# Optimization experiments

Measured on AMD Instinct MI355X. Metric: run time of the kernel, lower is better.

The kernel has to match this reference:

```python
import jax, jax.numpy as jnp
import numpy as np

BN_EPS = 1e-5
STRIDE = 12          # ACCENT_DOWNSAMPLE_STRIDE
NQ = 8               # ACCENT_VQ_QUANTIZERS
K = 256              # ACCENT_VQ_CODEBOOK_SIZE
VQ_D = 16            # ACCENT_VQ_DIM
EMB = 128            # ACCENT_EMBEDDING_DIM


def conv1d(x, w, b, stride=1, padding=0):
    # x: (B, Cin, T), w: (Cout, Cin, Kw)
    y = jax.lax.conv_general_dilated(
        x, w, window_strides=(stride,), padding=[(padding, padding)],
        dimension_numbers=("NCW", "OIW", "NCW"))
    return y + b[None, :, None]


def batchnorm(x, gamma, beta, mean, var):
    # eval-mode BatchNorm1d over channel dim
    inv = jax.lax.rsqrt(var + BN_EPS)
    return (x - mean[None, :, None]) * (inv * gamma)[None, :, None] + beta[None, :, None]


def setup_inputs() -> dict:
    key = jax.random.key(0)
    ks = jax.random.split(key, 12)
    C = 256
    d = {
        "mel_spectrogram": jax.random.normal(ks[0], (16, 80, 4096), jnp.float32),
        "w1": jax.random.normal(ks[1], (C, 80, 5), jnp.float32) * 0.05,
        "b1": jnp.zeros((C,), jnp.float32),
        "g1": jnp.ones((C,), jnp.float32),
        "be1": jnp.zeros((C,), jnp.float32),
        "m1": jax.random.normal(ks[2], (C,), jnp.float32) * 0.1,
        "v1": jax.random.uniform(ks[3], (C,), jnp.float32, 0.5, 1.5),
        "w2": jax.random.normal(ks[4], (C, C, 5), jnp.float32) * 0.03,
        "b2": jnp.zeros((C,), jnp.float32),
        "g2": jnp.ones((C,), jnp.float32),
        "be2": jnp.zeros((C,), jnp.float32),
        "m2": jax.random.normal(ks[5], (C,), jnp.float32) * 0.1,
        "v2": jax.random.uniform(ks[6], (C,), jnp.float32, 0.5, 1.5),
        "wd": jax.random.normal(ks[7], (EMB, C, 2 * STRIDE), jnp.float32) * 0.02,
        "bd": jnp.zeros((EMB,), jnp.float32),
        "wp": jax.random.normal(ks[8], (VQ_D, EMB, 1), jnp.float32) * 0.1,
        "bp": jnp.zeros((VQ_D,), jnp.float32),
        "codebooks": jax.random.normal(ks[9], (NQ, K, VQ_D), jnp.float32) * 0.3,
    }
    return d


def reference(mel_spectrogram, w1, b1, g1, be1, m1, v1,
              w2, b2, g2, be2, m2, v2, wd, bd, wp, bp, codebooks):
    # CNN stack
    x = jax.nn.relu(batchnorm(conv1d(mel_spectrogram, w1, b1, 1, 2), g1, be1, m1, v1))
    x = jax.nn.relu(batchnorm(conv1d(x, w2, b2, 1, 2), g2, be2, m2, v2))
    # Downsample conv: kernel=24, stride=12, pad=6
    e_a_unq = conv1d(x, wd, bd, STRIDE, STRIDE // 2)          # (B, 128, T')
    z = conv1d(e_a_unq, wp, bp, 1, 0)                          # (B, 16, T')
    # RVQ: 8 sequential cdist-argmin-subtract steps
    r = jnp.transpose(z, (0, 2, 1))                            # (B, T', 16)
    idx_list = []
    for q in range(NQ):
        cb = codebooks[q]                                      # (K, 16)
        # squared euclidean distances (B, T', K)
        d = (jnp.sum(r * r, -1, keepdims=True)
             - 2.0 * jnp.einsum("btd,kd->btk", r, cb)
             + jnp.sum(cb * cb, -1))
        idx = jnp.argmin(d, axis=-1)                           # (B, T')
        idx_list.append(idx)
        r = r - cb[idx]                                        # residual update
    indices = jnp.stack(idx_list, axis=0)                      # (NQ, B, T')
    return e_a_unq, indices
```

## Files before the change

kernel.cpp:

```cpp
#include <hip/hip_runtime.h>
#include <math.h>

#define B_    16
#define BCH   4
#define T_    4096
#define C_    256
#define CIN1  80
#define EMB   128
#define TP    341
#define NPOS  (B_*TP)
#define NQ_   8
#define KCB   256
#define BN_EPS 1e-5

__global__ __launch_bounds__(256) void prep_f64(
    const float* __restrict__ w1, const float* __restrict__ w2,
    const float* __restrict__ wd,
    const float* __restrict__ b1, const float* __restrict__ g1,
    const float* __restrict__ be1, const float* __restrict__ m1,
    const float* __restrict__ v1,
    const float* __restrict__ b2, const float* __restrict__ g2,
    const float* __restrict__ be2, const float* __restrict__ m2,
    const float* __restrict__ v2,
    const float* __restrict__ wp, const float* __restrict__ bp,
    double* __restrict__ w1t, double* __restrict__ w2t, double* __restrict__ wdt,
    double* __restrict__ a1, double* __restrict__ bt1,
    double* __restrict__ a2, double* __restrict__ bt2,
    double* __restrict__ wpd, double* __restrict__ bpd)
{
    int j = blockIdx.x * 256 + threadIdx.x;
    if (j < 256*24*128) wdt[j] = (double)wd[(size_t)(j & 127) * 6144 + (j >> 7)];
    if (j < 256*5*256)  w2t[j] = (double)w2[(size_t)(j & 255) * 1280 + (j >> 8)];
    if (j < 80*5*256)   w1t[j] = (double)w1[(size_t)(j & 255) * 400 + (j >> 8)];
    if (j < 16*128)     wpd[j] = (double)wp[j];
    if (j < 16)         bpd[j] = (double)bp[j];
    if (j < 256) {
        double inv1 = 1.0 / sqrt((double)v1[j] + BN_EPS);
        double s1 = (double)g1[j] * inv1;
        a1[j]  = s1;
        bt1[j] = ((double)b1[j] - (double)m1[j]) * s1 + (double)be1[j];
        double inv2 = 1.0 / sqrt((double)v2[j] + BN_EPS);
        double s2 = (double)g2[j] * inv2;
        a2[j]  = s2;
        bt2[j] = ((double)b2[j] - (double)m2[j]) * s2 + (double)be2[j];
    }
}

__device__ __forceinline__ int swz_pair(int col) {
    int bw = col >> 1;
    return ((bw ^ ((bw >> 3) & 7)) << 1);
}
__device__ __forceinline__ int swz_scalar(int col) {
    int bw = col >> 1;
    return (((bw ^ ((bw >> 3) & 7)) << 1) | (col & 1));
}

template<int CIN, typename Tin>
__global__ __launch_bounds__(256) void conv5_bn_relu_f64(
    const Tin* __restrict__ in,
    const double* __restrict__ wt,
    const double* __restrict__ alpha, const double* __restrict__ beta,
    double* __restrict__ out)
{
    const int b   = blockIdx.z;
    const int co0 = blockIdx.y * 64;
    const int t0  = blockIdx.x * 128;
    const int tid = threadIdx.x;
    const int tcol = tid & 15;
    const int trow = tid >> 4;

    __shared__ double xs[8][136];
    __shared__ double wsh[40][64];

    double acc[4][8];
    #pragma unroll
    for (int i = 0; i < 4; ++i)
        #pragma unroll
        for (int j = 0; j < 8; ++j) acc[i][j] = 0.0;

    for (int c0 = 0; c0 < CIN; c0 += 8) {
        for (int i = tid; i < 8 * 132; i += 256) {
            int ci = i / 132, col = i % 132;
            int t = t0 - 2 + col;
            double v = 0.0;
            if (t >= 0 && t < T_) v = (double)in[((size_t)(b * CIN + c0 + ci)) * T_ + t];
            xs[ci][swz_scalar(col)] = v;
        }
        for (int i = tid; i < 40 * 64; i += 256) {
            int r = i >> 6, co = i & 63;
            wsh[r][co] = wt[(size_t)(c0 * 5 + r) * 256 + co0 + co];
        }
        __syncthreads();

        #pragma unroll
        for (int ci = 0; ci < 8; ++ci) {
            double xv[12];
            #pragma unroll
            for (int m = 0; m < 6; ++m) {
                double2 v = *(const double2*)&xs[ci][swz_pair(tcol * 8 + 2 * m)];
                xv[2 * m] = v.x; xv[2 * m + 1] = v.y;
            }
            #pragma unroll
            for (int k = 0; k < 5; ++k) {
                double w0 = wsh[ci * 5 + k][trow * 4 + 0];
                double w1v = wsh[ci * 5 + k][trow * 4 + 1];
                double w2v = wsh[ci * 5 + k][trow * 4 + 2];
                double w3v = wsh[ci * 5 + k][trow * 4 + 3];
                #pragma unroll
                for (int j = 0; j < 8; ++j) {
                    double xq = xv[j + k];
                    acc[0][j] = fma(w0, xq, acc[0][j]);
                    acc[1][j] = fma(w1v, xq, acc[1][j]);
                    acc[2][j] = fma(w2v, xq, acc[2][j]);
                    acc[3][j] = fma(w3v, xq, acc[3][j]);
                }
            }
        }
        __syncthreads();
    }

    const int cobase = co0 + trow * 4;
    const int tg = t0 + tcol * 8;
    #pragma unroll
    for (int i = 0; i < 4; ++i) {
        double a = alpha[cobase + i], bt = beta[cobase + i];
        size_t base = ((size_t)(b * C_ + cobase + i)) * T_ + tg;
        #pragma unroll
        for (int j = 0; j < 8; ++j) {
            double y = fma(acc[i][j], a, bt);
            out[base + j] = y > 0.0 ? y : 0.0;
        }
    }
}

__global__ __launch_bounds__(256) void convd_f64_v6(
    const double* __restrict__ x2,
    const double* __restrict__ wdt,
    double* __restrict__ parts,
    int nb, int nsplit, int cis)
{
    const int bz  = blockIdx.z;
    const int s   = bz % nsplit;
    const int b   = bz / nsplit;
    const int tp0 = blockIdx.x * 64;
    const int tid = threadIdx.x;
    const int tcol = tid & 15;
    const int crow = tid >> 4;

    __shared__ double xs2[2][24][66];
    __shared__ double wsh[48][128];

    double acc[8][4];
    #pragma unroll
    for (int i = 0; i < 8; ++i)
        #pragma unroll
        for (int j = 0; j < 4; ++j) acc[i][j] = 0.0;

    const int tbase = tp0 * 12 - 6;
    const int ci_begin = s * cis;

    for (int c0 = ci_begin; c0 < ci_begin + cis; c0 += 2) {
        for (int i = tid; i < 2 * 780; i += 256) {
            int ci = i / 780, c = i % 780;
            int t = tbase + c;
            double v = (t >= 0 && t < T_)
                ? x2[((size_t)(b * 256 + c0 + ci)) * T_ + t] : 0.0;
            int tp = c / 12, kp = c % 12;
            xs2[ci][kp][tp] = v;
            if (tp >= 1) xs2[ci][kp + 12][tp - 1] = v;
        }
        for (int i = tid; i < 48 * 128; i += 256) {
            int r = i >> 7, c = i & 127;
            wsh[r][c] = wdt[(size_t)(c0 * 24 + r) * 128 + c];
        }
        __syncthreads();

        const double* xb = &xs2[0][0][0] + tcol;
        const double* wb = &wsh[0][0] + crow * 8;
        #pragma unroll
        for (int ci = 0; ci < 2; ++ci) {
            #pragma unroll
            for (int k = 0; k < 24; ++k) {
                double wv[8], xv[4];
                #pragma unroll
                for (int i = 0; i < 8; ++i) wv[i] = wb[(ci * 24 + k) * 128 + i];
                #pragma unroll
                for (int j = 0; j < 4; ++j) xv[j] = xb[(ci * 24 + k) * 66 + 16 * j];
                #pragma unroll
                for (int i = 0; i < 8; ++i)
                    #pragma unroll
                    for (int j = 0; j < 4; ++j)
                        acc[i][j] = fma(wv[i], xv[j], acc[i][j]);
            }
        }
        __syncthreads();
    }

    #pragma unroll
    for (int i = 0; i < 8; ++i) {
        int co = crow * 8 + i;
        #pragma unroll
        for (int j = 0; j < 4; ++j) {
            int tp = tp0 + tcol + 16 * j;
            if (tp < TP)
                parts[(((size_t)s * nb + b) * EMB + co) * TP + tp] = acc[i][j];
        }
    }
}

__global__ __launch_bounds__(256) void convd_combine(
    const double* __restrict__ parts,
    const float* __restrict__ bd,
    double* __restrict__ ed,
    float* __restrict__ e_out,
    int nb, int b_off, int nsplit)
{
    int idx = blockIdx.x * 256 + threadIdx.x;
    int total = nb * EMB * TP;
    if (idx >= total) return;
    int b_local = idx / (EMB * TP);
    int rem = idx % (EMB * TP);
    int co = rem / TP;
    size_t stride = (size_t)nb * EMB * TP;
    double y = 0.0;
    for (int s = 0; s < nsplit; ++s)
        y += parts[(size_t)s * stride + idx];
    y += (double)bd[co];
    size_t o = (size_t)(b_off + b_local) * EMB * TP + rem;
    ed[o] = y;
    e_out[o] = (float)y;
}

__global__ __launch_bounds__(128) void zproj_f64(
    const double* __restrict__ ed,
    const double* __restrict__ wpd,
    const double* __restrict__ bpd,
    double* __restrict__ z)
{
    const int b = blockIdx.y;
    const int t = blockIdx.x * 128 + threadIdx.x;
    __shared__ double wps[16][128];
    for (int i = threadIdx.x; i < 16 * 128; i += 128)
        wps[i >> 7][i & 127] = wpd[i];
    __syncthreads();
    if (t >= TP) return;
    double acc[16];
    #pragma unroll
    for (int v = 0; v < 16; ++v) acc[v] = bpd[v];
    for (int co = 0; co < 128; ++co) {
        double x = ed[((size_t)(b * EMB + co)) * TP + t];
        #pragma unroll
        for (int v = 0; v < 16; ++v) acc[v] = fma(x, wps[v][co], acc[v]);
    }
    #pragma unroll
    for (int v = 0; v < 16; ++v)
        z[((size_t)(b * TP + t)) * 16 + v] = acc[v];
}

__global__ __launch_bounds__(256) void rvq_f64_v2(
    const double* __restrict__ z,
    const float* __restrict__ cb,
    float* __restrict__ out_idx)
{
    const int pos = blockIdx.x;
    const int tid = threadIdx.x;
    const int lane = tid & 63;
    const int wv = tid >> 6;

    __shared__ double r[16];
    __shared__ double wd_s[4];
    __shared__ int wi_s[4];
    __shared__ int best_s;

    if (tid < 16) r[tid] = z[(size_t)pos * 16 + tid];
    __syncthreads();

    for (int q = 0; q < NQ_; ++q) {
        const float* c = cb + ((size_t)(q * KCB) + tid) * 16;
        double d = 0.0;
        #pragma unroll
        for (int i = 0; i < 16; ++i) {
            double diff = r[i] - (double)c[i];
            d = fma(diff, diff, d);
        }
        int idx = tid;
        #pragma unroll
        for (int sft = 32; sft > 0; sft >>= 1) {
            double d2 = __shfl_down(d, sft, 64);
            int i2 = __shfl_down(idx, sft, 64);
            if (d2 < d || (d2 == d && i2 < idx)) { d = d2; idx = i2; }
        }
        if (lane == 0) { wd_s[wv] = d; wi_s[wv] = idx; }
        __syncthreads();
        if (tid == 0) {
            double bd_ = wd_s[0]; int bi = wi_s[0];
            #pragma unroll
            for (int w = 1; w < 4; ++w) {
                if (wd_s[w] < bd_ || (wd_s[w] == bd_ && wi_s[w] < bi)) {
                    bd_ = wd_s[w]; bi = wi_s[w];
                }
            }
            best_s = bi;
            out_idx[(size_t)q * NPOS + pos] = (float)bi;
        }
        __syncthreads();
        int best = best_s;
        if (tid < 16)
            r[tid] = r[tid] - (double)cb[((size_t)(q * KCB) + best) * 16 + tid];
        __syncthreads();
    }
}

extern "C" void kernel_launch(void* const* d_in, const int* in_sizes, int n_in,
                              void* d_out, int out_size, void* d_ws, size_t ws_size,
                              hipStream_t stream) {
    const float* mel = (const float*)d_in[0];
    const float* w1  = (const float*)d_in[1];
    const float* b1  = (const float*)d_in[2];
    const float* g1  = (const float*)d_in[3];
    const float* be1 = (const float*)d_in[4];
    const float* m1  = (const float*)d_in[5];
    const float* v1  = (const float*)d_in[6];
    const float* w2  = (const float*)d_in[7];
    const float* b2  = (const float*)d_in[8];
    const float* g2  = (const float*)d_in[9];
    const float* be2 = (const float*)d_in[10];
    const float* m2  = (const float*)d_in[11];
    const float* v2  = (const float*)d_in[12];
    const float* wd  = (const float*)d_in[13];
    const float* bd  = (const float*)d_in[14];
    const float* wp  = (const float*)d_in[15];
    const float* bp  = (const float*)d_in[16];
    const float* cb  = (const float*)d_in[17];

    const int nb = 8;
    const int ngrp = B_ / nb;

    const size_t x1_bytes    = (size_t)BCH * C_ * T_ * 8;
    const size_t x2_bytes    = (size_t)nb * C_ * T_ * 8;
    const size_t fixed_bytes = x2_bytes + (size_t)80*5*256*8 + (size_t)256*5*256*8
                             + (size_t)256*24*128*8 + 4*2048 + 16384 + 256
                             + (size_t)16 * EMB * TP * 8
                             + (size_t)16 * TP * 16 * 8
                             + 16384;
    auto parts_bytes = [&](int ns) -> size_t {
        return (size_t)ns * nb * EMB * TP * 8;
    };
    auto need = [&](int ns) -> size_t {
        size_t shared = x1_bytes > parts_bytes(ns) ? x1_bytes : parts_bytes(ns);
        return shared + fixed_bytes;
    };
    int nsplit = (ws_size >= need(16)) ? 16 : 8;
    const int cis = 256 / nsplit;
    const size_t shared_bytes =
        x1_bytes > parts_bytes(nsplit) ? x1_bytes : parts_bytes(nsplit);

    char* ws = (char*)d_ws;
    size_t off = 0;
    auto alloc = [&](size_t bytes) -> char* {
        char* p = ws + off;
        off = (off + bytes + 255) & ~(size_t)255;
        return p;
    };
    char* shared = alloc(shared_bytes);
    double* x1d  = (double*)shared;
    double* parts= (double*)shared;
    double* x2d  = (double*)alloc(x2_bytes);
    double* w1td = (double*)alloc((size_t)80*5*256*8);
    double* w2td = (double*)alloc((size_t)256*5*256*8);
    double* wdtd = (double*)alloc((size_t)256*24*128*8);
    double* a1d  = (double*)alloc(2048);
    double* bt1d = (double*)alloc(2048);
    double* a2d  = (double*)alloc(2048);
    double* bt2d = (double*)alloc(2048);
    double* wpd  = (double*)alloc(16*128*8);
    double* bpd  = (double*)alloc(16*8);
    double* ed   = (double*)alloc((size_t)16 * EMB * TP * 8);
    double* zd   = (double*)alloc((size_t)16 * TP * 16 * 8);

    float* e_out   = (float*)d_out;
    float* idx_out = (float*)d_out + (size_t)B_ * EMB * TP;

    prep_f64<<<3072, 256, 0, stream>>>(w1, w2, wd, b1, g1, be1, m1, v1,
                                       b2, g2, be2, m2, v2, wp, bp,
                                       w1td, w2td, wdtd, a1d, bt1d, a2d, bt2d,
                                       wpd, bpd);

    const int comb_blocks = (nb * EMB * TP + 255) / 256;
    for (int g = 0; g < ngrp; ++g) {
        for (int ch = 0; ch < nb / BCH; ++ch) {
            int ch_abs = g * (nb / BCH) + ch;
            const float* mel_c = mel + (size_t)ch_abs * BCH * CIN1 * T_;
            conv5_bn_relu_f64<CIN1, float><<<dim3(32, 4, BCH), 256, 0, stream>>>(
                mel_c, w1td, a1d, bt1d, x1d);
            conv5_bn_relu_f64<C_, double><<<dim3(32, 4, BCH), 256, 0, stream>>>(
                x1d, w2td, a2d, bt2d, x2d + (size_t)ch * BCH * C_ * T_);
        }
        convd_f64_v6<<<dim3(6, 1, nb * nsplit), 256, 0, stream>>>(
            x2d, wdtd, parts, nb, nsplit, cis);
        convd_combine<<<comb_blocks, 256, 0, stream>>>(parts, bd, ed, e_out,
                                                       nb, g * nb, nsplit);
    }
    zproj_f64<<<dim3(3, 16), 128, 0, stream>>>(ed, wpd, bpd, zd);
    rvq_f64_v2<<<NPOS, 256, 0, stream>>>(zd, cb, idx_out);
}
```

Baseline: 1.876 ms.

## Keep weights in fp32, drop intermediate ed buffer, batch conv launches by workspace

Conv and projection weights now stay fp32 in global memory and are widened to double only when loaded into shared memory. w1 is read directly without a pre-transpose pass. The combine step writes reduced results in place into the partials buffer, and the z-projection then runs per group from that buffer, so the separate ed array is gone. When the workspace is large enough, each conv launch covers 8 batches instead of 4, and div/mod by 12 is replaced with a multiply-shift. The aim is less memory traffic, smaller prep work and fewer launches, at the cost of uncoalesced w1 loads and more complex workspace aliasing.

```diff
diff --git a/kernel.cpp b/kernel.cpp
--- a/kernel.cpp
+++ b/kernel.cpp
@@ -2,7 +2,6 @@
 #include <math.h>
 
 #define B_    16
-#define BCH   4
 #define T_    4096
 #define C_    256
 #define CIN1  80
@@ -13,27 +12,21 @@
 #define KCB   256
 #define BN_EPS 1e-5
 
-__global__ __launch_bounds__(256) void prep_f64(
-    const float* __restrict__ w1, const float* __restrict__ w2,
-    const float* __restrict__ wd,
+__global__ __launch_bounds__(256) void prep_v7(
+    const float* __restrict__ w2, const float* __restrict__ wd,
     const float* __restrict__ b1, const float* __restrict__ g1,
     const float* __restrict__ be1, const float* __restrict__ m1,
     const float* __restrict__ v1,
     const float* __restrict__ b2, const float* __restrict__ g2,
     const float* __restrict__ be2, const float* __restrict__ m2,
     const float* __restrict__ v2,
-    const float* __restrict__ wp, const float* __restrict__ bp,
-    double* __restrict__ w1t, double* __restrict__ w2t, double* __restrict__ wdt,
+    float* __restrict__ w2t, float* __restrict__ wdt,
     double* __restrict__ a1, double* __restrict__ bt1,
-    double* __restrict__ a2, double* __restrict__ bt2,
-    double* __restrict__ wpd, double* __restrict__ bpd)
+    double* __restrict__ a2, double* __restrict__ bt2)
 {
     int j = blockIdx.x * 256 + threadIdx.x;
-    if (j < 256*24*128) wdt[j] = (double)wd[(size_t)(j & 127) * 6144 + (j >> 7)];
-    if (j < 256*5*256)  w2t[j] = (double)w2[(size_t)(j & 255) * 1280 + (j >> 8)];
-    if (j < 80*5*256)   w1t[j] = (double)w1[(size_t)(j & 255) * 400 + (j >> 8)];
-    if (j < 16*128)     wpd[j] = (double)wp[j];
-    if (j < 16)         bpd[j] = (double)bp[j];
+    if (j < 256*24*128) wdt[j] = wd[(size_t)(j & 127) * 6144 + (j >> 7)];
+    if (j < 256*5*256)  w2t[j] = w2[(size_t)(j & 255) * 1280 + (j >> 8)];
     if (j < 256) {
         double inv1 = 1.0 / sqrt((double)v1[j] + BN_EPS);
         double s1 = (double)g1[j] * inv1;
@@ -55,10 +48,10 @@
     return (((bw ^ ((bw >> 3) & 7)) << 1) | (col & 1));
 }
 
-template<int CIN, typename Tin>
+template<int CIN, typename Tin, bool TR>
 __global__ __launch_bounds__(256) void conv5_bn_relu_f64(
     const Tin* __restrict__ in,
-    const double* __restrict__ wt,
+    const float* __restrict__ wt,
     const double* __restrict__ alpha, const double* __restrict__ beta,
     double* __restrict__ out)
 {
@@ -88,7 +81,10 @@
         }
         for (int i = tid; i < 40 * 64; i += 256) {
             int r = i >> 6, co = i & 63;
-            wsh[r][co] = wt[(size_t)(c0 * 5 + r) * 256 + co0 + co];
+            float wv;
+            if (TR) wv = wt[(size_t)(c0 * 5 + r) * 256 + co0 + co];
+            else    wv = wt[(size_t)(co0 + co) * (CIN * 5) + c0 * 5 + r];
+            wsh[r][co] = (double)wv;
         }
         __syncthreads();
 
@@ -135,7 +131,7 @@
 
 __global__ __launch_bounds__(256) void convd_f64_v6(
     const double* __restrict__ x2,
-    const double* __restrict__ wdt,
+    const float* __restrict__ wdt,
     double* __restrict__ parts,
     int nb, int nsplit, int cis)
 {
@@ -161,17 +157,19 @@
 
     for (int c0 = ci_begin; c0 < ci_begin + cis; c0 += 2) {
         for (int i = tid; i < 2 * 780; i += 256) {
-            int ci = i / 780, c = i % 780;
+            int ci = (i >= 780) ? 1 : 0;
+            int c = i - ci * 780;
             int t = tbase + c;
             double v = (t >= 0 && t < T_)
                 ? x2[((size_t)(b * 256 + c0 + ci)) * T_ + t] : 0.0;
-            int tp = c / 12, kp = c % 12;
+            int tp = (c * 43691) >> 19;
+            int kp = c - tp * 12;
             xs2[ci][kp][tp] = v;
             if (tp >= 1) xs2[ci][kp + 12][tp - 1] = v;
         }
         for (int i = tid; i < 48 * 128; i += 256) {
             int r = i >> 7, c = i & 127;
-            wsh[r][c] = wdt[(size_t)(c0 * 24 + r) * 128 + c];
+            wsh[r][c] = (double)wdt[(size_t)(c0 * 24 + r) * 128 + c];
         }
         __syncthreads();
 
@@ -209,44 +207,42 @@
 }
 
 __global__ __launch_bounds__(256) void convd_combine(
-    const double* __restrict__ parts,
+    double* __restrict__ parts,
     const float* __restrict__ bd,
-    double* __restrict__ ed,
     float* __restrict__ e_out,
     int nb, int b_off, int nsplit)
 {
     int idx = blockIdx.x * 256 + threadIdx.x;
     int total = nb * EMB * TP;
     if (idx >= total) return;
-    int b_local = idx / (EMB * TP);
     int rem = idx % (EMB * TP);
     int co = rem / TP;
+    int b_local = idx / (EMB * TP);
     size_t stride = (size_t)nb * EMB * TP;
     double y = 0.0;
     for (int s = 0; s < nsplit; ++s)
         y += parts[(size_t)s * stride + idx];
     y += (double)bd[co];
-    size_t o = (size_t)(b_off + b_local) * EMB * TP + rem;
-    ed[o] = y;
-    e_out[o] = (float)y;
+    parts[idx] = y;
+    e_out[(size_t)b_off * EMB * TP + idx] = (float)y;
 }
 
 __global__ __launch_bounds__(128) void zproj_f64(
     const double* __restrict__ ed,
-    const double* __restrict__ wpd,
-    const double* __restrict__ bpd,
+    const float* __restrict__ wp,
+    const float* __restrict__ bp,
     double* __restrict__ z)
 {
     const int b = blockIdx.y;
     const int t = blockIdx.x * 128 + threadIdx.x;
     __shared__ double wps[16][128];
     for (int i = threadIdx.x; i < 16 * 128; i += 128)
-        wps[i >> 7][i & 127] = wpd[i];
+        wps[i >> 7][i & 127] = (double)wp[i];
     __syncthreads();
     if (t >= TP) return;
     double acc[16];
     #pragma unroll
-    for (int v = 0; v < 16; ++v) acc[v] = bpd[v];
+    for (int v = 0; v < 16; ++v) acc[v] = (double)bp[v];
     for (int co = 0; co < 128; ++co) {
         double x = ed[((size_t)(b * EMB + co)) * TP + t];
         #pragma unroll
@@ -335,25 +331,24 @@
 
     const int nb = 8;
     const int ngrp = B_ / nb;
-
-    const size_t x1_bytes    = (size_t)BCH * C_ * T_ * 8;
-    const size_t x2_bytes    = (size_t)nb * C_ * T_ * 8;
-    const size_t fixed_bytes = x2_bytes + (size_t)80*5*256*8 + (size_t)256*5*256*8
-                             + (size_t)256*24*128*8 + 4*2048 + 16384 + 256
-                             + (size_t)16 * EMB * TP * 8
-                             + (size_t)16 * TP * 16 * 8
-                             + 16384;
-    auto parts_bytes = [&](int ns) -> size_t {
-        return (size_t)ns * nb * EMB * TP * 8;
-    };
-    auto need = [&](int ns) -> size_t {
-        size_t shared = x1_bytes > parts_bytes(ns) ? x1_bytes : parts_bytes(ns);
-        return shared + fixed_bytes;
-    };
-    int nsplit = (ws_size >= need(16)) ? 16 : 8;
+    const int nsplit = 16;
     const int cis = 256 / nsplit;
-    const size_t shared_bytes =
-        x1_bytes > parts_bytes(nsplit) ? x1_bytes : parts_bytes(nsplit);
+
+    auto al = [](size_t x) { return (x + 255) & ~(size_t)255; };
+    const size_t x1_big   = (size_t)nb * C_ * T_ * 8;
+    const size_t x1_small = (size_t)4  * C_ * T_ * 8;
+    const size_t parts_b  = (size_t)nsplit * nb * EMB * TP * 8;
+    const size_t x2_bytes = (size_t)nb * C_ * T_ * 8;
+    const size_t tail = al((size_t)256*5*256*4)
+                      + al((size_t)256*24*128*4)
+                      + 4 * al(2048)
+                      + al((size_t)B_ * TP * 16 * 8);
+    const size_t need_big = al(x1_big) + al(x2_bytes) + tail;
+
+    const bool big = (ws_size >= need_big);
+    const int cc = big ? 8 : 4;
+    const size_t shared_bytes = big ? x1_big
+                                    : (x1_small > parts_b ? x1_small : parts_b);
 
     char* ws = (char*)d_ws;
     size_t off = 0;
@@ -366,41 +361,40 @@
     double* x1d  = (double*)shared;
     double* parts= (double*)shared;
     double* x2d  = (double*)alloc(x2_bytes);
-    double* w1td = (double*)alloc((size_t)80*5*256*8);
-    double* w2td = (double*)alloc((size_t)256*5*256*8);
-    double* wdtd = (double*)alloc((size_t)256*24*128*8);
+    float*  w2t  = (float*)alloc((size_t)256*5*256*4);
+    float*  wdt  = (float*)alloc((size_t)256*24*128*4);
     double* a1d  = (double*)alloc(2048);
     double* bt1d = (double*)alloc(2048);
     double* a2d  = (double*)alloc(2048);
     double* bt2d = (double*)alloc(2048);
-    double* wpd  = (double*)alloc(16*128*8);
-    double* bpd  = (double*)alloc(16*8);
-    double* ed   = (double*)alloc((size_t)16 * EMB * TP * 8);
-    double* zd   = (double*)alloc((size_t)16 * TP * 16 * 8);
+    double* zd   = (double*)alloc((size_t)B_ * TP * 16 * 8);
 
     float* e_out   = (float*)d_out;
     float* idx_out = (float*)d_out + (size_t)B_ * EMB * TP;
 
-    prep_f64<<<3072, 256, 0, stream>>>(w1, w2, wd, b1, g1, be1, m1, v1,
-                                       b2, g2, be2, m2, v2, wp, bp,
-                                       w1td, w2td, wdtd, a1d, bt1d, a2d, bt2d,
-                                       wpd, bpd);
+    prep_v7<<<3072, 256, 0, stream>>>(w2, wd, b1, g1, be1, m1, v1,
+                                      b2, g2, be2, m2, v2,
+                                      w2t, wdt, a1d, bt1d, a2d, bt2d);
 
     const int comb_blocks = (nb * EMB * TP + 255) / 256;
     for (int g = 0; g < ngrp; ++g) {
-        for (int ch = 0; ch < nb / BCH; ++ch) {
-            int ch_abs = g * (nb / BCH) + ch;
-            const float* mel_c = mel + (size_t)ch_abs * BCH * CIN1 * T_;
-            conv5_bn_relu_f64<CIN1, float><<<dim3(32, 4, BCH), 256, 0, stream>>>(
-                mel_c, w1td, a1d, bt1d, x1d);
-            conv5_bn_relu_f64<C_, double><<<dim3(32, 4, BCH), 256, 0, stream>>>(
-                x1d, w2td, a2d, bt2d, x2d + (size_t)ch * BCH * C_ * T_);
+        for (int ch = 0; ch < nb / cc; ++ch) {
+            int b_abs = g * nb + ch * cc;
+            conv5_bn_relu_f64<CIN1, float, false>
+                <<<dim3(32, 4, cc), 256, 0, stream>>>(
+                mel + (size_t)b_abs * CIN1 * T_, w1, a1d, bt1d,
+                x1d + (big ? (size_t)ch * cc * C_ * T_ : 0));
+            conv5_bn_relu_f64<C_, double, true>
+                <<<dim3(32, 4, cc), 256, 0, stream>>>(
+                x1d + (big ? (size_t)ch * cc * C_ * T_ : 0), w2t, a2d, bt2d,
+                x2d + (size_t)ch * cc * C_ * T_);
         }
         convd_f64_v6<<<dim3(6, 1, nb * nsplit), 256, 0, stream>>>(
-            x2d, wdtd, parts, nb, nsplit, cis);
-        convd_combine<<<comb_blocks, 256, 0, stream>>>(parts, bd, ed, e_out,
-                                                       nb, g * nb, nsplit);
-    }
-    zproj_f64<<<dim3(3, 16), 128, 0, stream>>>(ed, wpd, bpd, zd);
+            x2d, wdt, parts, nb, nsplit, cis);
+        convd_combine<<<comb_blocks, 256, 0, stream>>>(
+            parts, bd, e_out, nb, g * nb, nsplit);
+        zproj_f64<<<dim3(3, nb), 128, 0, stream>>>(
+            parts, wp, bp, zd + (size_t)g * nb * TP * 16);
+    }
     rvq_f64_v2<<<NPOS, 256, 0, stream>>>(zd, cb, idx_out);
 }
```

After: 1.902 ms. No clear change (+1.3%).
